# Kernel tuning notes

Hardware: AMD Instinct MI355X
Metric: run time of the kernel (lower is better)

Reference implementation:

```python
import jax, jax.numpy as jnp
import numpy as np

C_IN, SEQ_LEN, K, G = 12, 8192, 8, 64
DIVISOR = 2 if G > 1 else 1
_G = G // DIVISOR
MAX_EXP = int(np.log2((SEQ_LEN - 1) / (9 - 1)))
DILATIONS = [2 ** e for e in range(MAX_EXP + 1)]   # 10 dilations for seq_len=8192
PADDINGS = [(9 - 1) * d // 2 for d in DILATIONS]
C_IN_PER = int(np.clip(C_IN // 2, 2, 8))
BATCH = 32


def _normalize(W):
    # zero-mean, L1-normalized over the kernel taps (last dim)
    W = W - W.mean(-1, keepdims=True)
    return W / jnp.abs(W).sum(-1, keepdims=True)


def setup_inputs() -> dict:
    key = jax.random.key(0)
    kx, kw, ki = jax.random.split(key, 3)
    X = jax.random.normal(kx, (BATCH, C_IN, SEQ_LEN), dtype=jnp.float32)
    # W: (num_dilations, divisor, k*_g, 1, 9) grouped-conv kernels
    W = _normalize(jax.random.normal(kw, (len(DILATIONS), DIVISOR, K * _G, 1, 9), dtype=jnp.float32))
    # I: (num_dilations, divisor, _g, c_in_per) channel-gather indices
    I = jax.random.randint(ki, (len(DILATIONS), DIVISOR, _G, C_IN_PER), 0, C_IN)
    return {"X": X, "W": W, "I": I}


def _branch(inp, Wd, d, p):
    # inp: (bs, _G, L); Wd: (K*_G, 1, 9); grouped dilated conv, 1 in-ch -> K out-ch per group
    z = jax.lax.conv_general_dilated(
        inp, Wd, window_strides=(1,), padding=[(p, p)], rhs_dilation=(d,),
        dimension_numbers=("NCH", "OIH", "NCH"), feature_group_count=_G)
    bs = inp.shape[0]
    z = z.reshape(bs, _G, K, -1)                      # (bs, _G, K, L)
    max_vals = z.max(axis=2)                          # (bs, _G, L)
    max_idx = z.argmax(axis=2)
    min_idx = z.argmin(axis=2)
    # histogram over K bins: sum of max values at argmax bin; count at argmin bin
    cmax = jnp.stack([jnp.where(max_idx == i, max_vals, 0.0).sum(-1) for i in range(K)], axis=-1)
    cmin = jnp.stack([(min_idx == i).astype(inp.dtype).sum(-1) for i in range(K)], axis=-1)
    return cmax, cmin                                 # each (bs, _G, K)


def reference(X, W, I):
    diff_X = jnp.diff(X, axis=-1)
    Z = []
    for di, (d, p) in enumerate(zip(DILATIONS, PADDINGS)):
        for j in range(min(2, G)):
            src = X if j == 0 else diff_X
            inp = src[:, I[di, j]].sum(2)             # gather channels, sum -> (bs, _G, L)
            cmax, cmin = _branch(inp, W[di, j], d, p)
            Z.append(cmax)
            Z.append(cmin)
    Z = jnp.concatenate(Z, axis=1)                    # (bs, 4*num_dilations*_G, K)
    return jax.nn.relu(Z)
```

## Files before the change

kernel.cpp:

```cpp
#include <hip/hip_runtime.h>


typedef __fp16 h2_t __attribute__((ext_vector_type(2)));

#define NB    32
#define CIN   12
#define SEQ   8192
#define NG    32
#define CPER  6
#define OUTCH 1280
#define XS_FLOATS 7736
#define GRID  10240

#define MAX3F(a, b, c) ({ float _r; asm("v_max3_f32 %0, %1, %2, %3" \
    : "=v"(_r) : "v"(a), "v"(b), "v"(c)); _r; })
#define MIN3F(a, b, c) ({ float _r; asm("v_min3_f32 %0, %1, %2, %3" \
    : "=v"(_r) : "v"(a), "v"(b), "v"(c)); _r; })

template <int DI>
__device__ __forceinline__ void hydra_body(
    const float* __restrict__ X, const float* __restrict__ W,
    const int* __restrict__ I, float* __restrict__ out,
    float* Xs, float* Smx, int j, int b, int chunk) {

  constexpr int d   = 1 << DI;
  constexpr int R   = (d < 16) ? d : 16;
  constexpr int rb  = (DI < 4) ? DI : 4;
  constexpr int Mm  = SEQ / d;
  constexpr int TMc = 512 / R;
  constexpr int TM  = (TMc < Mm) ? TMc : Mm;
  constexpr int MC  = Mm / TM;
  constexpr int RC  = d / R;
  constexpr int NR  = (RC * MC) / 16;
  constexpr int SR  = TM + 8;
  constexpr int CS  = R * SR + 4;
  constexpr int CL  = (R >= 8) ? TM : (TM * R / 8);
  constexpr int REP = (R == 16) ? 2 : 1;

  const int L = SEQ - j;
  const int tid = threadIdx.x;
  const int g = tid >> 3, s = tid & 7;

  h2_t Wp[8][4];
  float Wt[8];
  {
    const float* wp = W + (size_t)((DI * 2 + j) * 256 + g * 8) * 9;
#pragma unroll
    for (int k = 0; k < 8; ++k) {
#pragma unroll
      for (int t = 0; t < 4; ++t)
        Wp[k][t] = __builtin_amdgcn_cvt_pkrtz(wp[k * 9 + 2 * t], wp[k * 9 + 2 * t + 1]);
      Wt[k] = wp[k * 9 + 8];
    }
  }
  const float* base[CPER];
  {
    const int* ip = I + ((DI * 2 + j) * NG + g) * CPER;
#pragma unroll
    for (int i = 0; i < CPER; ++i) base[i] = Xs + ip[i] * CS;
  }

#pragma unroll
  for (int k = 0; k < 8; ++k) Smx[k * 256 + tid] = 0.f;

  unsigned long long cmnp = 0ull;

  for (int n = 0; n < NR; ++n) {
    const int cidx = chunk + 16 * n;
    const int rc = cidx & (RC - 1);
    const int mc = cidx / RC;
    const int r0 = rc * R;
    const int m0 = mc * TM;

    if (NR > 1 && n) __syncthreads();

    {
      const float* xb0 = X + (size_t)b * CIN * SEQ;
      if (j == 0) {
        for (int f = tid; f < R * SR; f += 256) {
          int rr = f & (R - 1), mm = f >> rb, mp = m0 + mm - 4;
          int pos = r0 + rr + mp * d;
          bool ok = (mp >= 0) && (pos < L);
          int lo = rr * SR + mm;
          const float* xp = xb0 + pos;
#pragma unroll
          for (int ch = 0; ch < CIN; ++ch) {
            Xs[ch * CS + lo] = ok ? xp[0] : 0.f;
            xp += SEQ;
          }
        }
      } else {
        for (int f = tid; f < R * SR; f += 256) {
          int rr = f & (R - 1), mm = f >> rb, mp = m0 + mm - 4;
          int pos = r0 + rr + mp * d;
          bool ok = (mp >= 0) && (pos < L);
          int lo = rr * SR + mm;
          const float* xp = xb0 + pos;
#pragma unroll
          for (int ch = 0; ch < CIN; ++ch) {
            Xs[ch * CS + lo] = ok ? (xp[1] - xp[0]) : 0.f;
            xp += SEQ;
          }
        }
      }
    }
    __syncthreads();

#pragma unroll
    for (int rep = 0; rep < REP; ++rep) {
      int rr = (R == 16) ? (s + (rep << 3)) : (s & (R - 1));
      int mst = (R >= 8) ? 0 : ((s >> rb) * CL);
      int rowoff = rr * SR + mst;

      auto ldsum = [&](int idx) {
        float4 r = *reinterpret_cast<const float4*>(base[0] + idx);
#pragma unroll
        for (int i = 1; i < CPER; ++i) {
          float4 t = *reinterpret_cast<const float4*>(base[i] + idx);
          r.x += t.x; r.y += t.y; r.z += t.z; r.w += t.w;
        }
        return r;
      };

      float4 w0 = ldsum(rowoff);
      float4 w1 = ldsum(rowoff + 4);
      float4 nw0 = ldsum(rowoff + 8);
      float4 nw1 = ldsum(rowoff + 12);
#pragma unroll 1
      for (int st = 0; st < CL; st += 8) {
        float4 w2 = nw0;
        float4 w3 = nw1;
        nw0 = ldsum(rowoff + st + 16);
        nw1 = ldsum(rowoff + st + 20);
        float xv[16] = {w0.x, w0.y, w0.z, w0.w,
                        w1.x, w1.y, w1.z, w1.w,
                        w2.x, w2.y, w2.z, w2.w,
                        w3.x, w3.y, w3.z, w3.w};
        h2_t E[8], O[7];
#pragma unroll
        for (int i = 0; i < 8; ++i)
          E[i] = __builtin_amdgcn_cvt_pkrtz(xv[2 * i], xv[2 * i + 1]);
#pragma unroll
        for (int i = 0; i < 7; ++i)
          O[i] = __builtin_amdgcn_cvt_pkrtz(xv[2 * i + 1], xv[2 * i + 2]);
#pragma unroll
        for (int p = 0; p < 8; ++p) {
          const h2_t* P = (p & 1) ? (O + (p >> 1)) : (E + (p >> 1));
          float tail = xv[8 + p];
          float zp[8];
#pragma unroll
          for (int k = 0; k < 8; ++k) {
            float a0 = Wt[k] * tail;
            a0 = __builtin_amdgcn_fdot2(Wp[k][3], P[3], a0, false);
            a0 = __builtin_amdgcn_fdot2(Wp[k][2], P[2], a0, false);
            a0 = __builtin_amdgcn_fdot2(Wp[k][1], P[1], a0, false);
            a0 = __builtin_amdgcn_fdot2(Wp[k][0], P[0], a0, false);
            zp[k] = __uint_as_float((__float_as_uint(a0) & 0xFFFFFFF8u) | (unsigned)k);
          }
          float t1 = MAX3F(zp[0], zp[1], zp[2]);
          float t2 = MAX3F(zp[3], zp[4], zp[5]);
          float t3 = MAX3F(zp[6], zp[7], t1);
          float mxp = fmaxf(t2, t3);
          float u1 = MIN3F(zp[0], zp[1], zp[2]);
          float u2 = MIN3F(zp[3], zp[4], zp[5]);
          float u3 = MIN3F(zp[6], zp[7], u1);
          float mnp = fminf(u2, u3);
          unsigned mxb = __float_as_uint(mxp);
          Smx[((mxb & 7u) << 8) + tid] += mxp;
          unsigned mnb = __float_as_uint(mnp);
          cmnp += 1ull << ((mnb & 7u) << 3);
        }
        w0 = w2; w1 = w3;
      }
    }
  }

  __syncthreads();

  {
    int cbase = (DI * 2 + j) * 64;
    float sum = 0.f;
#pragma unroll
    for (int s2 = 0; s2 < 8; ++s2) sum += Smx[(s << 8) + (g << 3) + s2];
    atomicAdd(out + ((size_t)b * OUTCH + cbase + g) * 8 + s, sum);

    int cnts[8];
#pragma unroll
    for (int k = 0; k < 8; ++k) cnts[k] = (int)((cmnp >> (k * 8)) & 0xFFull);
#pragma unroll
    for (int k = 0; k < 8; ++k) {
#pragma unroll
      for (int off = 1; off < 8; off <<= 1)
        cnts[k] += __shfl_xor(cnts[k], off);
    }
    int vn = cnts[0];
#pragma unroll
    for (int k = 1; k < 8; ++k) vn = (s == k) ? cnts[k] : vn;
    atomicAdd(out + ((size_t)b * OUTCH + cbase + 32 + g) * 8 + s, (float)vn);
  }
}

__global__ __launch_bounds__(256, 3) void hydra_fused(
    const float* __restrict__ X, const float* __restrict__ W,
    const int* __restrict__ I, float* __restrict__ out) {
  __shared__ float Xs[XS_FLOATS];
  __shared__ float Smx[2048];
  int u = blockIdx.x;
  int dj = u % 20;
  int rest = u / 20;
  int b = rest & 31;
  int chunk = rest >> 5;
  int j = dj & 1;
  switch (dj >> 1) {
    case 0: hydra_body<0>(X, W, I, out, Xs, Smx, j, b, chunk); break;
    case 1: hydra_body<1>(X, W, I, out, Xs, Smx, j, b, chunk); break;
    case 2: hydra_body<2>(X, W, I, out, Xs, Smx, j, b, chunk); break;
    case 3: hydra_body<3>(X, W, I, out, Xs, Smx, j, b, chunk); break;
    case 4: hydra_body<4>(X, W, I, out, Xs, Smx, j, b, chunk); break;
    case 5: hydra_body<5>(X, W, I, out, Xs, Smx, j, b, chunk); break;
    case 6: hydra_body<6>(X, W, I, out, Xs, Smx, j, b, chunk); break;
    case 7: hydra_body<7>(X, W, I, out, Xs, Smx, j, b, chunk); break;
    case 8: hydra_body<8>(X, W, I, out, Xs, Smx, j, b, chunk); break;
    case 9: hydra_body<9>(X, W, I, out, Xs, Smx, j, b, chunk); break;
  }
}

__global__ void hydra_relu(float* __restrict__ out, int n) {
  int i = blockIdx.x * 256 + threadIdx.x;
  if (i < n) out[i] = fmaxf(out[i], 0.f);
}

extern "C" void kernel_launch(void* const* d_in, const int* in_sizes, int n_in,
                              void* d_out, int out_size, void* d_ws, size_t ws_size,
                              hipStream_t stream) {
  const float* X = (const float*)d_in[0];
  const float* W = (const float*)d_in[1];
  const int*   I = (const int*)d_in[2];
  float* out = (float*)d_out;

  (void)hipMemsetAsync(d_out, 0, (size_t)out_size * sizeof(float), stream);
  hydra_fused<<<GRID, 256, 0, stream>>>(X, W, I, out);
  hydra_relu<<<(out_size + 255) / 256, 256, 0, stream>>>(out, out_size);
}
```

Measured before the change: 445.7 us.

## Segment LDS rows for small dilations to reduce bank conflicts; drop load prefetch

For dilations with fewer than 8 residue rows, the shared-memory tile is reorganized into 64-element segments, each with its own 8-element halo, stored at a stride of 76 floats. Each thread therefore reads from its own padded segment instead of from contiguous offsets that likely collide on LDS banks. The staging loop is rewritten to fill these segments, which loads halo elements redundantly. The software prefetch of the next window (nw0/nw1) is also removed, which cuts register pressure but exposes LDS latency inside the inner loop.

```diff
diff --git a/kernel.cpp b/kernel.cpp
--- a/kernel.cpp
+++ b/kernel.cpp
@@ -9,7 +9,7 @@
 #define NG    32
 #define CPER  6
 #define OUTCH 1280
-#define XS_FLOATS 7736
+#define XS_FLOATS 7728
 #define GRID  10240
 
 #define MAX3F(a, b, c) ({ float _r; asm("v_max3_f32 %0, %1, %2, %3" \
@@ -32,7 +32,10 @@
   constexpr int MC  = Mm / TM;
   constexpr int RC  = d / R;
   constexpr int NR  = (RC * MC) / 16;
-  constexpr int SR  = TM + 8;
+  constexpr int CPR = (R < 8) ? (TM / 64) : 1;
+  constexpr int CB  = (R < 8) ? ((TM == 512) ? 3 : (TM == 256) ? 2 : 1) : 0;
+  constexpr int SEG = 76;
+  constexpr int SR  = (R < 8) ? (CPR * SEG) : (TM + 8);
   constexpr int CS  = R * SR + 4;
   constexpr int CL  = (R >= 8) ? TM : (TM * R / 8);
   constexpr int REP = (R == 16) ? 2 : 1;
@@ -76,7 +79,33 @@
 
     {
       const float* xb0 = X + (size_t)b * CIN * SEQ;
-      if (j == 0) {
+      if (R < 8) {
+        constexpr int NSTG = R * CPR * 72;
+        for (int f = tid; f < NSTG; f += 256) {
+          int within = f % 72;
+          int q = f / 72;
+          int c = q & (CPR - 1);
+          int rr = q >> CB;
+          int mp = m0 + (c << 6) + within - 4;
+          int pos = r0 + rr + mp * d;
+          bool ok = (mp >= 0) && (pos < L);
+          int lo = rr * SR + c * SEG + within;
+          const float* xp = xb0 + pos;
+          if (j == 0) {
+#pragma unroll
+            for (int ch = 0; ch < CIN; ++ch) {
+              Xs[ch * CS + lo] = ok ? xp[0] : 0.f;
+              xp += SEQ;
+            }
+          } else {
+#pragma unroll
+            for (int ch = 0; ch < CIN; ++ch) {
+              Xs[ch * CS + lo] = ok ? (xp[1] - xp[0]) : 0.f;
+              xp += SEQ;
+            }
+          }
+        }
+      } else if (j == 0) {
         for (int f = tid; f < R * SR; f += 256) {
           int rr = f & (R - 1), mm = f >> rb, mp = m0 + mm - 4;
           int pos = r0 + rr + mp * d;
@@ -109,8 +138,8 @@
 #pragma unroll
     for (int rep = 0; rep < REP; ++rep) {
       int rr = (R == 16) ? (s + (rep << 3)) : (s & (R - 1));
-      int mst = (R >= 8) ? 0 : ((s >> rb) * CL);
-      int rowoff = rr * SR + mst;
+      int rowoff = (R < 8) ? (rr * SR + (s >> rb) * SEG)
+                           : (rr * SR);
 
       auto ldsum = [&](int idx) {
         float4 r = *reinterpret_cast<const float4*>(base[0] + idx);
@@ -124,14 +153,10 @@
 
       float4 w0 = ldsum(rowoff);
       float4 w1 = ldsum(rowoff + 4);
-      float4 nw0 = ldsum(rowoff + 8);
-      float4 nw1 = ldsum(rowoff + 12);
 #pragma unroll 1
       for (int st = 0; st < CL; st += 8) {
-        float4 w2 = nw0;
-        float4 w3 = nw1;
-        nw0 = ldsum(rowoff + st + 16);
-        nw1 = ldsum(rowoff + st + 20);
+        float4 w2 = ldsum(rowoff + st + 8);
+        float4 w3 = ldsum(rowoff + st + 12);
         float xv[16] = {w0.x, w0.y, w0.z, w0.w,
                         w1.x, w1.y, w1.z, w1.w,
                         w2.x, w2.y, w2.z, w2.w,
```

Measured after the change: 421.6 us. 5.4% less time.
